# Optimization experiments

Measured on AMD Instinct MI355X. Metric: run time of the kernel, lower is better.

Reference implementation:

```python
import jax, jax.numpy as jnp
import numpy as np


def setup_inputs() -> dict:
    key = jax.random.key(0)
    ks = jax.random.split(key, 4)
    B, C, T = 4, 256, 4096
    Cq = C // 8
    x = jax.random.normal(ks[0], (B, C, T), dtype=jnp.float32)
    Wq = jax.random.normal(ks[1], (Cq, C), dtype=jnp.float32) * (1.0 / np.sqrt(C))
    Wk = jax.random.normal(ks[2], (Cq, C), dtype=jnp.float32) * (1.0 / np.sqrt(C))
    Wv = jax.random.normal(ks[3], (C, C), dtype=jnp.float32) * (1.0 / np.sqrt(C))
    bq = jnp.zeros((Cq,), dtype=jnp.float32)
    bk = jnp.zeros((Cq,), dtype=jnp.float32)
    bv = jnp.zeros((C,), dtype=jnp.float32)
    return {"x": x, "Wq": Wq, "bq": bq, "Wk": Wk, "bk": bk, "Wv": Wv, "bv": bv}


def reference(x, Wq, bq, Wk, bk, Wv, bv):
    # x: [B, C, T]; 1x1 conv == per-timestep linear over channels
    q = jnp.einsum('oc,bct->bto', Wq, x) + bq          # [B, T, Cq]  (proj_query permuted)
    k = jnp.einsum('oc,bct->bot', Wk, x) + bk[:, None]  # [B, Cq, T]
    v = jnp.einsum('oc,bct->bot', Wv, x) + bv[:, None]  # [B, C, T]
    attn = jax.nn.softmax(jnp.einsum('bto,bos->bts', q, k), axis=-1)  # [B, T, T]
    out = jnp.einsum('bcs,bts->bct', v, attn)           # V @ attn^T
    return out + x
```

## Files before the change

### kernel.cpp

```cpp
#include <hip/hip_runtime.h>
#include <hip/hip_bf16.h>

#define BB 4
#define CC 256
#define TT 4096
#define CQ 32
#define LOG2E 1.44269504088896340736f

typedef __bf16 bf16;
typedef __bf16 bf16x4 __attribute__((ext_vector_type(4)));
typedef __bf16 bf16x8 __attribute__((ext_vector_type(8)));
typedef float floatx4 __attribute__((ext_vector_type(4)));

#define MFMA16(a, b, c) __builtin_amdgcn_mfma_f32_16x16x32_bf16(a, b, c, 0, 0, 0)

__device__ __forceinline__ void gload_lds16(const void* g, void* l) {
    __builtin_amdgcn_global_load_lds(
        (const __attribute__((address_space(1))) void*)g,
        (__attribute__((address_space(3))) void*)l, 16, 0, 0);
}

__device__ __forceinline__ void lgkm_barrier() {
    asm volatile("s_waitcnt lgkmcnt(0)" ::: "memory");
    __builtin_amdgcn_s_barrier();
    asm volatile("" ::: "memory");
}

__global__ __launch_bounds__(256) void wconv_kernel(
    const float* __restrict__ Wq, const float* __restrict__ Wk,
    const float* __restrict__ Wv, bf16* __restrict__ Wb)
{
    int i = (blockIdx.x * 256 + threadIdx.x) * 4;
    float4 v;
    if (i < 8192)       v = *(const float4*)(Wq + i);
    else if (i < 16384) v = *(const float4*)(Wk + (i - 8192));
    else                v = *(const float4*)(Wv + (i - 16384));
    bf16x4 o;
    o[0] = (bf16)v.x; o[1] = (bf16)v.y; o[2] = (bf16)v.z; o[3] = (bf16)v.w;
    *(bf16x4*)(Wb + i) = o;
}

__global__ __launch_bounds__(256) void xt_kernel(const float* __restrict__ x,
                                                 float* __restrict__ xT)
{
    __shared__ float tile[64][65];
    const int tid = threadIdx.x;
    const int tb = blockIdx.x * 64, cb = blockIdx.y * 64, b = blockIdx.z;
    const int rr = tid >> 4;
    const int q4 = (tid & 15) * 4;
    #pragma unroll
    for (int p = 0; p < 4; ++p) {
        int c = p * 16 + rr;
        float4 v = *(const float4*)(x + ((size_t)(b * CC + cb + c)) * TT + tb + q4);
        tile[c][q4 + 0] = v.x; tile[c][q4 + 1] = v.y;
        tile[c][q4 + 2] = v.z; tile[c][q4 + 3] = v.w;
    }
    __syncthreads();
    #pragma unroll
    for (int p = 0; p < 4; ++p) {
        int t = p * 16 + rr;
        float4 o;
        o.x = tile[q4 + 0][t]; o.y = tile[q4 + 1][t];
        o.z = tile[q4 + 2][t]; o.w = tile[q4 + 3][t];
        *(float4*)(xT + ((size_t)(b * TT + tb + t)) * CC + cb + q4) = o;
    }
}

__global__ __launch_bounds__(256) void proj_kernel(
    const float* __restrict__ xT, const bf16* __restrict__ Wb,
    const float* __restrict__ bq, const float* __restrict__ bk,
    const float* __restrict__ bv,
    bf16* __restrict__ Qo, bf16* __restrict__ Ko, bf16* __restrict__ Vo)
{
    const int tid  = threadIdx.x;
    const int lane = tid & 63, w = tid >> 6;
    const int l15  = lane & 15, quad = lane >> 4;
    const int b    = blockIdx.y;
    const int t    = blockIdx.x * 64 + w * 16 + l15;

    const bf16* Wqb = Wb;
    const bf16* Wkb = Wb + 8192;
    const bf16* Wvb = Wb + 16384;
    const float* xrow = xT + ((size_t)(b * TT + t)) * CC;

    floatx4 aq[2] = {}, ak[2] = {}, av[16] = {};
    for (int k = 0; k < 8; ++k) {
        float4 xa = *(const float4*)(xrow + k * 32 + quad * 8);
        float4 xc = *(const float4*)(xrow + k * 32 + quad * 8 + 4);
        bf16x8 xf;
        xf[0] = (bf16)xa.x; xf[1] = (bf16)xa.y; xf[2] = (bf16)xa.z; xf[3] = (bf16)xa.w;
        xf[4] = (bf16)xc.x; xf[5] = (bf16)xc.y; xf[6] = (bf16)xc.z; xf[7] = (bf16)xc.w;
        #pragma unroll
        for (int mt = 0; mt < 2; ++mt) {
            bf16x8 a0 = *(const bf16x8*)(Wqb + (size_t)(mt * 16 + l15) * CC + k * 32 + quad * 8);
            aq[mt] = MFMA16(a0, xf, aq[mt]);
            bf16x8 a1 = *(const bf16x8*)(Wkb + (size_t)(mt * 16 + l15) * CC + k * 32 + quad * 8);
            ak[mt] = MFMA16(a1, xf, ak[mt]);
        }
        #pragma unroll
        for (int vm = 0; vm < 16; ++vm) {
            bf16x8 a = *(const bf16x8*)(Wvb + (size_t)(vm * 16 + l15) * CC + k * 32 + quad * 8);
            av[vm] = MFMA16(a, xf, av[vm]);
        }
    }

    #pragma unroll
    for (int mt = 0; mt < 2; ++mt) {
        float4 bsq = *(const float4*)(bq + mt * 16 + quad * 4);
        float4 bsk = *(const float4*)(bk + mt * 16 + quad * 4);
        bf16x4 vq, vk;
        vq[0] = (bf16)((aq[mt][0] + bsq.x) * LOG2E);
        vq[1] = (bf16)((aq[mt][1] + bsq.y) * LOG2E);
        vq[2] = (bf16)((aq[mt][2] + bsq.z) * LOG2E);
        vq[3] = (bf16)((aq[mt][3] + bsq.w) * LOG2E);
        vk[0] = (bf16)(ak[mt][0] + bsk.x);
        vk[1] = (bf16)(ak[mt][1] + bsk.y);
        vk[2] = (bf16)(ak[mt][2] + bsk.z);
        vk[3] = (bf16)(ak[mt][3] + bsk.w);
        *(bf16x4*)(Qo + ((size_t)(b * TT + t)) * CQ + mt * 16 + quad * 4) = vq;
        *(bf16x4*)(Ko + ((size_t)(b * TT + t)) * CQ + mt * 16 + quad * 4) = vk;
    }
    #pragma unroll
    for (int vm = 0; vm < 16; ++vm) {
        float4 bs = *(const float4*)(bv + vm * 16 + quad * 4);
        #pragma unroll
        for (int r = 0; r < 4; ++r)
            Vo[((size_t)(b * CC + vm * 16 + quad * 4 + r)) * TT + t] =
                (bf16)(av[vm][r] + ((const float*)&bs)[r]);
    }
}

__global__ __launch_bounds__(256, 2) void flash_kernel(
    const bf16* __restrict__ Q, const bf16* __restrict__ K,
    const bf16* __restrict__ V, float* __restrict__ Op, float* __restrict__ lp)
{
    __shared__ __align__(16) char smem[65536 + 8192];
    char* Psb = smem + 65536;

    const int tid  = threadIdx.x;
    const int t0   = blockIdx.x * 64;
    const int sp   = blockIdx.y, b = blockIdx.z;
    const int lane = tid & 63, w = tid >> 6;
    const int l15  = lane & 15, quad = lane >> 4;
    const size_t sbase = (size_t)sp * (TT / 2);

    const bf16x8 qf = *(const bf16x8*)(
        Q + ((size_t)b * TT + t0 + w * 16 + l15) * CQ + quad * 8);

    const bf16* Kb = K + ((size_t)b * TT + sbase) * CQ;

    const int vchunk = (lane & 7) ^ (lane >> 3);
    const bf16* vsrc[8];
    #pragma unroll
    for (int i = 0; i < 8; ++i) {
        int c = w * 64 + i * 8 + (lane >> 3);
        vsrc[i] = V + ((size_t)(b * CC + c)) * TT + sbase + vchunk * 8;
    }

    floatx4 acc[4][4] = {};
    float lsum[4] = {};

    bf16x8 kfc[4];
    #pragma unroll
    for (int nt = 0; nt < 4; ++nt)
        kfc[nt] = *(const bf16x8*)(Kb + (size_t)(nt * 16 + l15) * CQ + quad * 8);

    #pragma unroll
    for (int i = 0; i < 8; ++i)
        gload_lds16(vsrc[i], smem + w * 8192 + i * 1024);

    asm volatile("s_waitcnt vmcnt(0)" ::: "memory");

    for (int st = 0; st < 32; ++st) {
        const int p = st & 1;
        if (st + 1 < 32) {
            #pragma unroll
            for (int i = 0; i < 8; ++i)
                gload_lds16(vsrc[i] + (size_t)(st + 1) * 64,
                            smem + (p ^ 1) * 32768 + w * 8192 + i * 1024);
        }

        floatx4 sc[4];
        #pragma unroll
        for (int nt = 0; nt < 4; ++nt) {
            floatx4 z = {};
            sc[nt] = MFMA16(qf, kfc[nt], z);
        }

        const int prow = w * 16 + quad * 4;
        #pragma unroll
        for (int nt = 0; nt < 4; ++nt)
            #pragma unroll
            for (int r = 0; r < 4; ++r) {
                float pv = __builtin_amdgcn_exp2f(sc[nt][r]);
                lsum[r] += pv;
                int row  = prow + r;
                int s    = nt * 16 + l15;
                int slot = (s >> 3) ^ (row & 7);
                *(bf16*)(Psb + row * 128 + slot * 16 + (s & 7) * 2) = (bf16)pv;
            }
        lgkm_barrier();

        bf16x8 pa[4][2];
        #pragma unroll
        for (int mt = 0; mt < 4; ++mt) {
            int row = mt * 16 + l15;
            #pragma unroll
            for (int kt = 0; kt < 2; ++kt) {
                int slot = (kt * 4 + quad) ^ (row & 7);
                pa[mt][kt] = *(const bf16x8*)(Psb + row * 128 + slot * 16);
            }
        }
        lgkm_barrier();

        if (st + 1 < 32) {
            #pragma unroll
            for (int nt = 0; nt < 4; ++nt)
                kfc[nt] = *(const bf16x8*)(
                    Kb + (size_t)((st + 1) * 64 + nt * 16 + l15) * CQ + quad * 8);
        }
        __builtin_amdgcn_s_setprio(1);
        #pragma unroll
        for (int kt = 0; kt < 2; ++kt)
            #pragma unroll
            for (int ntc = 0; ntc < 4; ++ntc) {
                int c    = w * 64 + ntc * 16 + l15;
                int slot = (kt * 4 + quad) ^ (l15 & 7);
                bf16x8 vf = *(const bf16x8*)(smem + p * 32768 + c * 128 + slot * 16);
                #pragma unroll
                for (int mt = 0; mt < 4; ++mt)
                    acc[mt][ntc] = MFMA16(pa[mt][kt], vf, acc[mt][ntc]);
            }
        __builtin_amdgcn_s_setprio(0);
    }

    #pragma unroll
    for (int r = 0; r < 4; ++r) {
        float s = lsum[r];
        s += __shfl_xor(s, 1); s += __shfl_xor(s, 2);
        s += __shfl_xor(s, 4); s += __shfl_xor(s, 8);
        lsum[r] = s;
    }

    float* op = Op + ((size_t)((sp * BB + b) * TT + t0)) * CC;
    #pragma unroll
    for (int mt = 0; mt < 4; ++mt)
        #pragma unroll
        for (int ntc = 0; ntc < 4; ++ntc)
            #pragma unroll
            for (int r = 0; r < 4; ++r)
                op[(size_t)(mt * 16 + quad * 4 + r) * CC + w * 64 + ntc * 16 + l15] =
                    acc[mt][ntc][r];
    if (l15 == 0) {
        #pragma unroll
        for (int r = 0; r < 4; ++r)
            lp[(size_t)(sp * BB + b) * TT + t0 + w * 16 + quad * 4 + r] = lsum[r];
    }
}

__global__ __launch_bounds__(256) void combine_kernel(
    const float* __restrict__ Op, const float* __restrict__ lp,
    const float* __restrict__ x, float* __restrict__ out)
{
    __shared__ float Os[32 * 260];
    __shared__ float Ls[32];
    const int tid = threadIdx.x;
    const int t0 = blockIdx.x * 32, b = blockIdx.y;

    if (tid < 32) {
        float l = lp[(size_t)b * TT + t0 + tid] + lp[(size_t)(BB + b) * TT + t0 + tid];
        Ls[tid] = 1.f / l;
    }
    const float* p0 = Op + ((size_t)(b * TT + t0)) * CC;
    const float* p1 = Op + ((size_t)((BB + b) * TT + t0)) * CC;
    #pragma unroll
    for (int it = 0; it < 8; ++it) {
        int chunk = it * 256 + tid;
        int t = chunk >> 6, c4 = (chunk & 63) * 4;
        float4 a = *(const float4*)(p0 + (size_t)t * CC + c4);
        float4 c2 = *(const float4*)(p1 + (size_t)t * CC + c4);
        Os[t * 260 + c4 + 0] = a.x + c2.x;
        Os[t * 260 + c4 + 1] = a.y + c2.y;
        Os[t * 260 + c4 + 2] = a.z + c2.z;
        Os[t * 260 + c4 + 3] = a.w + c2.w;
    }
    __syncthreads();

    const int tq = (tid & 7) * 4, crow = tid >> 3;
    #pragma unroll
    for (int pass = 0; pass < 8; ++pass) {
        int c = pass * 32 + crow;
        size_t base = ((size_t)(b * CC + c)) * TT + t0 + tq;
        float4 xr = *(const float4*)(x + base);
        float4 o;
        o.x = Os[(tq + 0) * 260 + c] * Ls[tq + 0] + xr.x;
        o.y = Os[(tq + 1) * 260 + c] * Ls[tq + 1] + xr.y;
        o.z = Os[(tq + 2) * 260 + c] * Ls[tq + 2] + xr.z;
        o.w = Os[(tq + 3) * 260 + c] * Ls[tq + 3] + xr.w;
        *(float4*)(out + base) = o;
    }
}

extern "C" void kernel_launch(void* const* d_in, const int* in_sizes, int n_in,
                              void* d_out, int out_size, void* d_ws, size_t ws_size,
                              hipStream_t stream) {
    const float* x  = (const float*)d_in[0];
    const float* Wq = (const float*)d_in[1];
    const float* bq = (const float*)d_in[2];
    const float* Wk = (const float*)d_in[3];
    const float* bk = (const float*)d_in[4];
    const float* Wv = (const float*)d_in[5];
    const float* bv = (const float*)d_in[6];
    float* out = (float*)d_out;

    char* ws = (char*)d_ws;
    bf16*  Wb = (bf16*)ws;
    bf16*  Qw = (bf16*)(ws + 163840);
    bf16*  Kw = (bf16*)(ws + 163840 + 1048576);
    bf16*  Vw = (bf16*)(ws + 163840 + 2097152);
    char*  R  = ws + 163840 + 2097152 + 8388608;
    float* xT = (float*)R;
    float* Op = (float*)R;
    float* lp = (float*)(R + 33554432);

    wconv_kernel<<<dim3(80), 256, 0, stream>>>(Wq, Wk, Wv, Wb);
    xt_kernel<<<dim3(64, 4, BB), 256, 0, stream>>>(x, xT);
    proj_kernel<<<dim3(64, BB), 256, 0, stream>>>(xT, Wb, bq, bk, bv, Qw, Kw, Vw);
    flash_kernel<<<dim3(64, 2, BB), 256, 0, stream>>>(Qw, Kw, Vw, Op, lp);
    combine_kernel<<<dim3(128, BB), 256, 0, stream>>>(Op, lp, x, out);
}
```

Baseline: 165.3 us.

## Split flash and projection work across more blocks; store transposed x as bf16

The flash kernel now gives each block half of the 256 output channels, so there are twice as many blocks, each with half the LDS and accumulators, and the occupancy hint rises from 2 to 4 blocks per CU. The projection kernel is split along a new grid dimension so each block computes 10 of the 20 output tiles. The transposed x buffer is stored as bf16 instead of fp32, which halves that traffic. The cost is that each flash block recomputes the QK^T scores and exp for its half, doubling that work across the grid.

```diff
diff --git a/kernel.cpp b/kernel.cpp
--- a/kernel.cpp
+++ b/kernel.cpp
@@ -41,7 +41,7 @@
 }
 
 __global__ __launch_bounds__(256) void xt_kernel(const float* __restrict__ x,
-                                                 float* __restrict__ xT)
+                                                 bf16* __restrict__ xT)
 {
     __shared__ float tile[64][65];
     const int tid = threadIdx.x;
@@ -59,15 +59,15 @@
     #pragma unroll
     for (int p = 0; p < 4; ++p) {
         int t = p * 16 + rr;
-        float4 o;
-        o.x = tile[q4 + 0][t]; o.y = tile[q4 + 1][t];
-        o.z = tile[q4 + 2][t]; o.w = tile[q4 + 3][t];
-        *(float4*)(xT + ((size_t)(b * TT + tb + t)) * CC + cb + q4) = o;
+        bf16x4 o;
+        o[0] = (bf16)tile[q4 + 0][t]; o[1] = (bf16)tile[q4 + 1][t];
+        o[2] = (bf16)tile[q4 + 2][t]; o[3] = (bf16)tile[q4 + 3][t];
+        *(bf16x4*)(xT + ((size_t)(b * TT + tb + t)) * CC + cb + q4) = o;
     }
 }
 
 __global__ __launch_bounds__(256) void proj_kernel(
-    const float* __restrict__ xT, const bf16* __restrict__ Wb,
+    const bf16* __restrict__ xT, const bf16* __restrict__ Wb,
     const float* __restrict__ bq, const float* __restrict__ bk,
     const float* __restrict__ bv,
     bf16* __restrict__ Qo, bf16* __restrict__ Ko, bf16* __restrict__ Vo)
@@ -76,69 +76,88 @@
     const int lane = tid & 63, w = tid >> 6;
     const int l15  = lane & 15, quad = lane >> 4;
     const int b    = blockIdx.y;
+    const int h    = blockIdx.z;
     const int t    = blockIdx.x * 64 + w * 16 + l15;
 
     const bf16* Wqb = Wb;
     const bf16* Wkb = Wb + 8192;
     const bf16* Wvb = Wb + 16384;
-    const float* xrow = xT + ((size_t)(b * TT + t)) * CC;
-
-    floatx4 aq[2] = {}, ak[2] = {}, av[16] = {};
+    const bf16* xrow = xT + ((size_t)(b * TT + t)) * CC;
+
+    const bf16* arow[10];
+    if (h == 0) {
+        arow[0] = Wqb + (size_t)l15 * CC;
+        arow[1] = Wqb + (size_t)(16 + l15) * CC;
+        arow[2] = Wkb + (size_t)l15 * CC;
+        arow[3] = Wkb + (size_t)(16 + l15) * CC;
+        #pragma unroll
+        for (int i = 0; i < 6; ++i)
+            arow[4 + i] = Wvb + (size_t)(i * 16 + l15) * CC;
+    } else {
+        #pragma unroll
+        for (int i = 0; i < 10; ++i)
+            arow[i] = Wvb + (size_t)(96 + i * 16 + l15) * CC;
+    }
+
+    floatx4 acc[10] = {};
     for (int k = 0; k < 8; ++k) {
-        float4 xa = *(const float4*)(xrow + k * 32 + quad * 8);
-        float4 xc = *(const float4*)(xrow + k * 32 + quad * 8 + 4);
-        bf16x8 xf;
-        xf[0] = (bf16)xa.x; xf[1] = (bf16)xa.y; xf[2] = (bf16)xa.z; xf[3] = (bf16)xa.w;
-        xf[4] = (bf16)xc.x; xf[5] = (bf16)xc.y; xf[6] = (bf16)xc.z; xf[7] = (bf16)xc.w;
+        bf16x8 xf = *(const bf16x8*)(xrow + k * 32 + quad * 8);
+        #pragma unroll
+        for (int j = 0; j < 10; ++j) {
+            bf16x8 a = *(const bf16x8*)(arow[j] + k * 32 + quad * 8);
+            acc[j] = MFMA16(a, xf, acc[j]);
+        }
+    }
+
+    if (h == 0) {
         #pragma unroll
         for (int mt = 0; mt < 2; ++mt) {
-            bf16x8 a0 = *(const bf16x8*)(Wqb + (size_t)(mt * 16 + l15) * CC + k * 32 + quad * 8);
-            aq[mt] = MFMA16(a0, xf, aq[mt]);
-            bf16x8 a1 = *(const bf16x8*)(Wkb + (size_t)(mt * 16 + l15) * CC + k * 32 + quad * 8);
-            ak[mt] = MFMA16(a1, xf, ak[mt]);
-        }
-        #pragma unroll
-        for (int vm = 0; vm < 16; ++vm) {
-            bf16x8 a = *(const bf16x8*)(Wvb + (size_t)(vm * 16 + l15) * CC + k * 32 + quad * 8);
-            av[vm] = MFMA16(a, xf, av[vm]);
-        }
-    }
-
-    #pragma unroll
-    for (int mt = 0; mt < 2; ++mt) {
-        float4 bsq = *(const float4*)(bq + mt * 16 + quad * 4);
-        float4 bsk = *(const float4*)(bk + mt * 16 + quad * 4);
-        bf16x4 vq, vk;
-        vq[0] = (bf16)((aq[mt][0] + bsq.x) * LOG2E);
-        vq[1] = (bf16)((aq[mt][1] + bsq.y) * LOG2E);
-        vq[2] = (bf16)((aq[mt][2] + bsq.z) * LOG2E);
-        vq[3] = (bf16)((aq[mt][3] + bsq.w) * LOG2E);
-        vk[0] = (bf16)(ak[mt][0] + bsk.x);
-        vk[1] = (bf16)(ak[mt][1] + bsk.y);
-        vk[2] = (bf16)(ak[mt][2] + bsk.z);
-        vk[3] = (bf16)(ak[mt][3] + bsk.w);
-        *(bf16x4*)(Qo + ((size_t)(b * TT + t)) * CQ + mt * 16 + quad * 4) = vq;
-        *(bf16x4*)(Ko + ((size_t)(b * TT + t)) * CQ + mt * 16 + quad * 4) = vk;
-    }
-    #pragma unroll
-    for (int vm = 0; vm < 16; ++vm) {
-        float4 bs = *(const float4*)(bv + vm * 16 + quad * 4);
-        #pragma unroll
-        for (int r = 0; r < 4; ++r)
-            Vo[((size_t)(b * CC + vm * 16 + quad * 4 + r)) * TT + t] =
-                (bf16)(av[vm][r] + ((const float*)&bs)[r]);
-    }
-}
-
-__global__ __launch_bounds__(256, 2) void flash_kernel(
+            float4 bsq = *(const float4*)(bq + mt * 16 + quad * 4);
+            float4 bsk = *(const float4*)(bk + mt * 16 + quad * 4);
+            bf16x4 vq, vk;
+            vq[0] = (bf16)((acc[mt][0] + bsq.x) * LOG2E);
+            vq[1] = (bf16)((acc[mt][1] + bsq.y) * LOG2E);
+            vq[2] = (bf16)((acc[mt][2] + bsq.z) * LOG2E);
+            vq[3] = (bf16)((acc[mt][3] + bsq.w) * LOG2E);
+            vk[0] = (bf16)(acc[2 + mt][0] + bsk.x);
+            vk[1] = (bf16)(acc[2 + mt][1] + bsk.y);
+            vk[2] = (bf16)(acc[2 + mt][2] + bsk.z);
+            vk[3] = (bf16)(acc[2 + mt][3] + bsk.w);
+            *(bf16x4*)(Qo + ((size_t)(b * TT + t)) * CQ + mt * 16 + quad * 4) = vq;
+            *(bf16x4*)(Ko + ((size_t)(b * TT + t)) * CQ + mt * 16 + quad * 4) = vk;
+        }
+        #pragma unroll
+        for (int vm = 0; vm < 6; ++vm) {
+            float4 bs = *(const float4*)(bv + vm * 16 + quad * 4);
+            #pragma unroll
+            for (int r = 0; r < 4; ++r)
+                Vo[((size_t)(b * CC + vm * 16 + quad * 4 + r)) * TT + t] =
+                    (bf16)(acc[4 + vm][r] + ((const float*)&bs)[r]);
+        }
+    } else {
+        #pragma unroll
+        for (int i = 0; i < 10; ++i) {
+            int vm = 6 + i;
+            float4 bs = *(const float4*)(bv + vm * 16 + quad * 4);
+            #pragma unroll
+            for (int r = 0; r < 4; ++r)
+                Vo[((size_t)(b * CC + vm * 16 + quad * 4 + r)) * TT + t] =
+                    (bf16)(acc[i][r] + ((const float*)&bs)[r]);
+        }
+    }
+}
+
+__global__ __launch_bounds__(256, 4) void flash_kernel(
     const bf16* __restrict__ Q, const bf16* __restrict__ K,
     const bf16* __restrict__ V, float* __restrict__ Op, float* __restrict__ lp)
 {
-    __shared__ __align__(16) char smem[65536 + 8192];
-    char* Psb = smem + 65536;
+    __shared__ __align__(16) char smem[32768 + 8192];
+    char* Psb = smem + 32768;
 
     const int tid  = threadIdx.x;
-    const int t0   = blockIdx.x * 64;
+    const int bx   = blockIdx.x;
+    const int t0   = (bx >> 1) * 64;
+    const int cb   = bx & 1;
     const int sp   = blockIdx.y, b = blockIdx.z;
     const int lane = tid & 63, w = tid >> 6;
     const int l15  = lane & 15, quad = lane >> 4;
@@ -150,14 +169,14 @@
     const bf16* Kb = K + ((size_t)b * TT + sbase) * CQ;
 
     const int vchunk = (lane & 7) ^ (lane >> 3);
-    const bf16* vsrc[8];
-    #pragma unroll
-    for (int i = 0; i < 8; ++i) {
-        int c = w * 64 + i * 8 + (lane >> 3);
+    const bf16* vsrc[4];
+    #pragma unroll
+    for (int i = 0; i < 4; ++i) {
+        int c = cb * 128 + w * 32 + i * 8 + (lane >> 3);
         vsrc[i] = V + ((size_t)(b * CC + c)) * TT + sbase + vchunk * 8;
     }
 
-    floatx4 acc[4][4] = {};
+    floatx4 acc[4][2] = {};
     float lsum[4] = {};
 
     bf16x8 kfc[4];
@@ -166,8 +185,8 @@
         kfc[nt] = *(const bf16x8*)(Kb + (size_t)(nt * 16 + l15) * CQ + quad * 8);
 
     #pragma unroll
-    for (int i = 0; i < 8; ++i)
-        gload_lds16(vsrc[i], smem + w * 8192 + i * 1024);
+    for (int i = 0; i < 4; ++i)
+        gload_lds16(vsrc[i], smem + w * 4096 + i * 1024);
 
     asm volatile("s_waitcnt vmcnt(0)" ::: "memory");
 
@@ -175,9 +194,9 @@
         const int p = st & 1;
         if (st + 1 < 32) {
             #pragma unroll
-            for (int i = 0; i < 8; ++i)
+            for (int i = 0; i < 4; ++i)
                 gload_lds16(vsrc[i] + (size_t)(st + 1) * 64,
-                            smem + (p ^ 1) * 32768 + w * 8192 + i * 1024);
+                            smem + (p ^ 1) * 16384 + w * 4096 + i * 1024);
         }
 
         floatx4 sc[4];
@@ -223,10 +242,10 @@
         #pragma unroll
         for (int kt = 0; kt < 2; ++kt)
             #pragma unroll
-            for (int ntc = 0; ntc < 4; ++ntc) {
-                int c    = w * 64 + ntc * 16 + l15;
+            for (int ntc = 0; ntc < 2; ++ntc) {
+                int cl   = w * 32 + ntc * 16 + l15;
                 int slot = (kt * 4 + quad) ^ (l15 & 7);
-                bf16x8 vf = *(const bf16x8*)(smem + p * 32768 + c * 128 + slot * 16);
+                bf16x8 vf = *(const bf16x8*)(smem + p * 16384 + cl * 128 + slot * 16);
                 #pragma unroll
                 for (int mt = 0; mt < 4; ++mt)
                     acc[mt][ntc] = MFMA16(pa[mt][kt], vf, acc[mt][ntc]);
@@ -246,12 +265,12 @@
     #pragma unroll
     for (int mt = 0; mt < 4; ++mt)
         #pragma unroll
-        for (int ntc = 0; ntc < 4; ++ntc)
+        for (int ntc = 0; ntc < 2; ++ntc)
             #pragma unroll
             for (int r = 0; r < 4; ++r)
-                op[(size_t)(mt * 16 + quad * 4 + r) * CC + w * 64 + ntc * 16 + l15] =
-                    acc[mt][ntc][r];
-    if (l15 == 0) {
+                op[(size_t)(mt * 16 + quad * 4 + r) * CC +
+                   cb * 128 + w * 32 + ntc * 16 + l15] = acc[mt][ntc][r];
+    if (cb == 0 && l15 == 0) {
         #pragma unroll
         for (int r = 0; r < 4; ++r)
             lp[(size_t)(sp * BB + b) * TT + t0 + w * 16 + quad * 4 + r] = lsum[r];
@@ -319,13 +338,13 @@
     bf16*  Kw = (bf16*)(ws + 163840 + 1048576);
     bf16*  Vw = (bf16*)(ws + 163840 + 2097152);
     char*  R  = ws + 163840 + 2097152 + 8388608;
-    float* xT = (float*)R;
+    bf16*  xT = (bf16*)R;
     float* Op = (float*)R;
     float* lp = (float*)(R + 33554432);
 
     wconv_kernel<<<dim3(80), 256, 0, stream>>>(Wq, Wk, Wv, Wb);
     xt_kernel<<<dim3(64, 4, BB), 256, 0, stream>>>(x, xT);
-    proj_kernel<<<dim3(64, BB), 256, 0, stream>>>(xT, Wb, bq, bk, bv, Qw, Kw, Vw);
-    flash_kernel<<<dim3(64, 2, BB), 256, 0, stream>>>(Qw, Kw, Vw, Op, lp);
+    proj_kernel<<<dim3(64, BB, 2), 256, 0, stream>>>(xT, Wb, bq, bk, bv, Qw, Kw, Vw);
+    flash_kernel<<<dim3(128, 2, BB), 256, 0, stream>>>(Qw, Kw, Vw, Op, lp);
     combine_kernel<<<dim3(128, BB), 256, 0, stream>>>(Op, lp, x, out);
 }
```

After: 176.7 us. 1.07x slower.
